# Optimization experiments

Hardware: AMD Instinct MI355X
Metric: run time of the kernel (lower is better)

The kernel has to match this reference:

```python
import jax, jax.numpy as jnp
import numpy as np

BS, SEQ, H = 64, 512, 768
E, T, K = 32, 64, 64


def setup_inputs() -> dict:
    key = jax.random.key(0)
    ks = jax.random.split(key, 16)
    return {
        "hidden_states": jax.random.normal(ks[0], (BS, SEQ, H), dtype=jnp.float32),
        "Wsrc": jax.random.normal(ks[1], (862, 384), dtype=jnp.float32) * 0.02,
        "Wtgt": jax.random.normal(ks[2], (862, 384), dtype=jnp.float32) * 0.02,
        "W_cls": jax.random.normal(ks[3], (2, 6144), dtype=jnp.float32) * 0.02,
        "b_cls": jnp.zeros((2,), dtype=jnp.float32),
        "W_topic": jax.random.normal(ks[4], (2, 6144), dtype=jnp.float32) * 0.02,
        "b_topic": jnp.zeros((2,), dtype=jnp.float32),
        "W_token": jax.random.normal(ks[5], (2, 6144), dtype=jnp.float32) * 0.02,
        "b_token": jnp.zeros((2,), dtype=jnp.float32),
        "source_ids": jax.random.randint(ks[6], (BS,), 0, 862),
        "target_ids": jax.random.randint(ks[7], (BS,), 0, 862),
        "ent_inds": jax.random.randint(ks[8], (BS, E), 0, SEQ - 1),
        "ent_mask": jnp.ones((BS, E), dtype=jnp.float32),
        "topic_inds": jax.random.randint(ks[9], (BS, T), 0, SEQ),
        "topic_mask": jnp.ones((BS, T), dtype=jnp.float32),
        "token_inds": jax.random.randint(ks[10], (BS, K), 0, SEQ),
        "token_mask": jnp.ones((BS, K), dtype=jnp.float32),
    }


def reference(hidden_states, Wsrc, Wtgt, W_cls, b_cls, W_topic, b_topic,
              W_token, b_token, source_ids, target_ids, ent_inds, ent_mask,
              topic_inds, topic_mask, token_inds, token_mask):
    bs = hidden_states.shape[0]
    # domain embedding: concat(source_emb, target_emb) -> [bs, 768] -> [bs, 96, 8]
    domain = jnp.concatenate([Wsrc[source_ids], Wtgt[target_ids]], axis=1)
    d0 = domain.reshape(bs, 96, 8)

    def gather(inds, mask, offset=0):
        # ragged gather of hidden states at token positions, zero-padded slots masked
        h = jnp.take_along_axis(hidden_states, (inds + offset)[:, :, None], axis=1)
        return h * mask[:, :, None]  # [bs, L, 768]

    ent_h = gather(ent_inds, ent_mask, offset=1)
    topic_h = gather(topic_inds, topic_mask)
    token_h = gather(token_inds, token_mask)

    # CLS bilinear: outer product over the 8-dim factor, [bs,96,8,8] -> [bs,6144]
    cls_h = hidden_states[:, 0, :].reshape(bs, 96, 8)
    bl_cls = (d0[:, :, :, None] * cls_h[:, :, None, :]).reshape(bs, 6144)
    cls_logits = jax.nn.softmax(bl_cls @ W_cls.T + b_cls, axis=1)

    def bilin(h, W, b):
        h4 = h.reshape(bs, -1, 96, 8)  # [bs, L, 96, 8]
        bl = (d0[:, None, :, :, None] * h4[:, :, :, None, :]).reshape(bs, h4.shape[1], 6144)
        return bl @ W.T + b  # [bs, L, n_out]

    topic_logits = jax.nn.softmax(bilin(topic_h, W_topic, b_topic), axis=2)
    token_logits = bilin(token_h, W_token, b_token)
    return cls_logits, topic_logits, token_logits
```

## Files before the change

### kernel.cpp

```cpp
#include <hip/hip_runtime.h>

#define BSZ 64
#define SEQ 512
#define HD  768
#define TT  64
#define NROW 6
#define NTASK 129

__global__ __launch_bounds__(256) void compute_V_kernel(
    const float* __restrict__ Wsrc,
    const float* __restrict__ Wtgt,
    const float* __restrict__ W_cls,
    const float* __restrict__ W_topic,
    const float* __restrict__ W_token,
    const int*   __restrict__ source_ids,
    const int*   __restrict__ target_ids,
    float*       __restrict__ Vg)
{
    __shared__ __align__(16) float dom[HD];
    const int b   = blockIdx.x;
    const int tid = threadIdx.x;

    const int sid = source_ids[b];
    const int tgt = target_ids[b];
    for (int j = tid; j < HD; j += 256)
        dom[j] = (j < 384) ? Wsrc[sid * 384 + j] : Wtgt[tgt * 384 + (j - 384)];
    __syncthreads();

    for (int idx = tid; idx < NROW * HD; idx += 256) {
        const int r = idx / HD;
        const int d = idx - r * HD;
        const int w = r >> 1, o = r & 1;
        const float* Wp = (w == 0) ? W_cls : (w == 1) ? W_topic : W_token;
        const int m = d >> 3, c = d & 7;
        const float* wrow = Wp + o * 6144 + m * 64 + c;
        float acc = 0.f;
        #pragma unroll
        for (int a = 0; a < 8; ++a)
            acc = fmaf(dom[m * 8 + a], wrow[a * 8], acc);
        Vg[(size_t)b * (NROW * HD) + idx] = acc;
    }
}

__global__ __launch_bounds__(256) void task_kernel(
    const float* __restrict__ hidden,
    const float* __restrict__ Vg,
    const float* __restrict__ b_cls,
    const float* __restrict__ b_topic,
    const float* __restrict__ b_token,
    const int*   __restrict__ topic_inds,
    const float* __restrict__ topic_mask,
    const int*   __restrict__ token_inds,
    const float* __restrict__ token_mask,
    float*       __restrict__ out)
{
    const int wg   = blockIdx.x * 4 + (threadIdx.x >> 6);
    const int lane = threadIdx.x & 63;
    const int b    = wg / NTASK;
    const int t    = wg - b * NTASK;

    int w, pos, outoff;
    float mask;
    const float* bias;
    bool do_softmax;
    if (t == 0) {
        w = 0; pos = 0; mask = 1.f; bias = b_cls; do_softmax = true;
        outoff = b * 2;
    } else if (t <= TT) {
        const int l = t - 1;
        w = 1; pos = topic_inds[b * TT + l]; mask = topic_mask[b * TT + l];
        bias = b_topic; do_softmax = true;
        outoff = 128 + (b * TT + l) * 2;
    } else {
        const int l = t - 1 - TT;
        w = 2; pos = token_inds[b * TT + l]; mask = token_mask[b * TT + l];
        bias = b_token; do_softmax = false;
        outoff = 128 + BSZ * TT * 2 + (b * TT + l) * 2;
    }

    const float4* hrow = reinterpret_cast<const float4*>(
        hidden + ((size_t)b * SEQ + (size_t)pos) * HD);
    const float4* v0 = reinterpret_cast<const float4*>(
        Vg + ((size_t)b * NROW + w * 2 + 0) * HD);
    const float4* v1 = reinterpret_cast<const float4*>(
        Vg + ((size_t)b * NROW + w * 2 + 1) * HD);

    float a0 = 0.f, a1 = 0.f;
    #pragma unroll
    for (int k = 0; k < 3; ++k) {
        const float4 h4 = hrow[lane + k * 64];
        const float4 x0 = v0[lane + k * 64];
        const float4 x1 = v1[lane + k * 64];
        a0 = fmaf(h4.x, x0.x, a0); a1 = fmaf(h4.x, x1.x, a1);
        a0 = fmaf(h4.y, x0.y, a0); a1 = fmaf(h4.y, x1.y, a1);
        a0 = fmaf(h4.z, x0.z, a0); a1 = fmaf(h4.z, x1.z, a1);
        a0 = fmaf(h4.w, x0.w, a0); a1 = fmaf(h4.w, x1.w, a1);
    }
    #pragma unroll
    for (int off = 32; off > 0; off >>= 1) {
        a0 += __shfl_down(a0, off, 64);
        a1 += __shfl_down(a1, off, 64);
    }

    if (lane == 0) {
        const float l0 = fmaf(mask, a0, bias[0]);
        const float l1 = fmaf(mask, a1, bias[1]);
        if (do_softmax) {
            const float mx = fmaxf(l0, l1);
            const float e0 = __expf(l0 - mx);
            const float e1 = __expf(l1 - mx);
            const float inv = 1.f / (e0 + e1);
            out[outoff]     = e0 * inv;
            out[outoff + 1] = e1 * inv;
        } else {
            out[outoff]     = l0;
            out[outoff + 1] = l1;
        }
    }
}

extern "C" void kernel_launch(void* const* d_in, const int* in_sizes, int n_in,
                              void* d_out, int out_size, void* d_ws, size_t ws_size,
                              hipStream_t stream) {
    const float* hidden     = (const float*)d_in[0];
    const float* Wsrc       = (const float*)d_in[1];
    const float* Wtgt       = (const float*)d_in[2];
    const float* W_cls      = (const float*)d_in[3];
    const float* b_cls      = (const float*)d_in[4];
    const float* W_topic    = (const float*)d_in[5];
    const float* b_topic    = (const float*)d_in[6];
    const float* W_token    = (const float*)d_in[7];
    const float* b_token    = (const float*)d_in[8];
    const int*   source_ids = (const int*)d_in[9];
    const int*   target_ids = (const int*)d_in[10];
    const int*   topic_inds = (const int*)d_in[13];
    const float* topic_mask = (const float*)d_in[14];
    const int*   token_inds = (const int*)d_in[15];
    const float* token_mask = (const float*)d_in[16];
    float* out = (float*)d_out;
    float* Vg  = (float*)d_ws;

    compute_V_kernel<<<BSZ, 256, 0, stream>>>(
        Wsrc, Wtgt, W_cls, W_topic, W_token, source_ids, target_ids, Vg);

    task_kernel<<<(BSZ * NTASK) / 4, 256, 0, stream>>>(
        hidden, Vg, b_cls, b_topic, b_token,
        topic_inds, topic_mask, token_inds, token_mask, out);
}
```

Measured before the change: 168.1 us.

## Fuse V computation and task dot-products into one kernel with shared-memory V

Merges the two kernels into a single launch of 512 blocks (8 partitions per batch item). Each block recomputes only the V rows it needs into shared memory, then runs its 16 or 17 gather-dot tasks against LDS instead of a global workspace. This removes one kernel launch, the global V write and read-back, and the serialisation between the two kernels. In exchange, V rows are computed redundantly across partitions and only 512 blocks exist versus the previous 2064, so there is less parallelism.

```diff
diff --git a/kernel.cpp b/kernel.cpp
--- a/kernel.cpp
+++ b/kernel.cpp
@@ -4,21 +4,33 @@
 #define SEQ 512
 #define HD  768
 #define TT  64
-#define NROW 6
-#define NTASK 129
+#define NPART 8
+#define TPP 16
 
-__global__ __launch_bounds__(256) void compute_V_kernel(
+__global__ __launch_bounds__(256) void fused_kernel(
+    const float* __restrict__ hidden,
     const float* __restrict__ Wsrc,
     const float* __restrict__ Wtgt,
     const float* __restrict__ W_cls,
     const float* __restrict__ W_topic,
     const float* __restrict__ W_token,
+    const float* __restrict__ b_cls,
+    const float* __restrict__ b_topic,
+    const float* __restrict__ b_token,
     const int*   __restrict__ source_ids,
     const int*   __restrict__ target_ids,
-    float*       __restrict__ Vg)
+    const int*   __restrict__ topic_inds,
+    const float* __restrict__ topic_mask,
+    const int*   __restrict__ token_inds,
+    const float* __restrict__ token_mask,
+    float*       __restrict__ out)
 {
     __shared__ __align__(16) float dom[HD];
-    const int b   = blockIdx.x;
+    __shared__ __align__(16) float Vl[4][HD];
+
+    const int blk = blockIdx.x;
+    const int b   = blk >> 3;
+    const int p   = blk & 7;
     const int tid = threadIdx.x;
 
     const int sid = source_ids[b];
@@ -27,10 +39,16 @@
         dom[j] = (j < 384) ? Wsrc[sid * 384 + j] : Wtgt[tgt * 384 + (j - 384)];
     __syncthreads();
 
-    for (int idx = tid; idx < NROW * HD; idx += 256) {
-        const int r = idx / HD;
-        const int d = idx - r * HD;
-        const int w = r >> 1, o = r & 1;
+    int base_row, nrows;
+    if (p == 0)      { base_row = 0; nrows = 4; }
+    else if (p < 4)  { base_row = 2; nrows = 2; }
+    else             { base_row = 4; nrows = 2; }
+
+    for (int idx = tid; idx < nrows * HD; idx += 256) {
+        const int ri = idx / HD;
+        const int d  = idx - ri * HD;
+        const int r  = base_row + ri;
+        const int w  = r >> 1, o = r & 1;
         const float* Wp = (w == 0) ? W_cls : (w == 1) ? W_topic : W_token;
         const int m = d >> 3, c = d & 7;
         const float* wrow = Wp + o * 6144 + m * 64 + c;
@@ -38,83 +56,72 @@
         #pragma unroll
         for (int a = 0; a < 8; ++a)
             acc = fmaf(dom[m * 8 + a], wrow[a * 8], acc);
-        Vg[(size_t)b * (NROW * HD) + idx] = acc;
+        Vl[ri][d] = acc;
     }
-}
+    __syncthreads();
 
-__global__ __launch_bounds__(256) void task_kernel(
-    const float* __restrict__ hidden,
-    const float* __restrict__ Vg,
-    const float* __restrict__ b_cls,
-    const float* __restrict__ b_topic,
-    const float* __restrict__ b_token,
-    const int*   __restrict__ topic_inds,
-    const float* __restrict__ topic_mask,
-    const int*   __restrict__ token_inds,
-    const float* __restrict__ token_mask,
-    float*       __restrict__ out)
-{
-    const int wg   = blockIdx.x * 4 + (threadIdx.x >> 6);
-    const int lane = threadIdx.x & 63;
-    const int b    = wg / NTASK;
-    const int t    = wg - b * NTASK;
+    const int wid  = tid >> 6;
+    const int lane = tid & 63;
+    const int ntasks = (p == 0) ? (1 + TPP) : TPP;
 
-    int w, pos, outoff;
-    float mask;
-    const float* bias;
-    bool do_softmax;
-    if (t == 0) {
-        w = 0; pos = 0; mask = 1.f; bias = b_cls; do_softmax = true;
-        outoff = b * 2;
-    } else if (t <= TT) {
-        const int l = t - 1;
-        w = 1; pos = topic_inds[b * TT + l]; mask = topic_mask[b * TT + l];
-        bias = b_topic; do_softmax = true;
-        outoff = 128 + (b * TT + l) * 2;
-    } else {
-        const int l = t - 1 - TT;
-        w = 2; pos = token_inds[b * TT + l]; mask = token_mask[b * TT + l];
-        bias = b_token; do_softmax = false;
-        outoff = 128 + BSZ * TT * 2 + (b * TT + l) * 2;
-    }
+    for (int ti = wid; ti < ntasks; ti += 4) {
+        int pos, outoff, vbase;
+        float mask;
+        const float* bias;
+        bool do_softmax;
+        if (p == 0 && ti == 0) {
+            pos = 0; mask = 1.f; bias = b_cls; do_softmax = true;
+            outoff = b * 2; vbase = 0;
+        } else if (p < 4) {
+            const int l = (p == 0) ? (ti - 1) : (p * TPP + ti);
+            pos = topic_inds[b * TT + l]; mask = topic_mask[b * TT + l];
+            bias = b_topic; do_softmax = true;
+            outoff = 128 + (b * TT + l) * 2;
+            vbase = (p == 0) ? 2 : 0;
+        } else {
+            const int l = (p - 4) * TPP + ti;
+            pos = token_inds[b * TT + l]; mask = token_mask[b * TT + l];
+            bias = b_token; do_softmax = false;
+            outoff = 128 + BSZ * TT * 2 + (b * TT + l) * 2;
+            vbase = 0;
+        }
 
-    const float4* hrow = reinterpret_cast<const float4*>(
-        hidden + ((size_t)b * SEQ + (size_t)pos) * HD);
-    const float4* v0 = reinterpret_cast<const float4*>(
-        Vg + ((size_t)b * NROW + w * 2 + 0) * HD);
-    const float4* v1 = reinterpret_cast<const float4*>(
-        Vg + ((size_t)b * NROW + w * 2 + 1) * HD);
+        const float4* hrow = reinterpret_cast<const float4*>(
+            hidden + ((size_t)b * SEQ + (size_t)pos) * HD);
+        const float4* v0 = reinterpret_cast<const float4*>(&Vl[vbase][0]);
+        const float4* v1 = reinterpret_cast<const float4*>(&Vl[vbase + 1][0]);
 
-    float a0 = 0.f, a1 = 0.f;
-    #pragma unroll
-    for (int k = 0; k < 3; ++k) {
-        const float4 h4 = hrow[lane + k * 64];
-        const float4 x0 = v0[lane + k * 64];
-        const float4 x1 = v1[lane + k * 64];
-        a0 = fmaf(h4.x, x0.x, a0); a1 = fmaf(h4.x, x1.x, a1);
-        a0 = fmaf(h4.y, x0.y, a0); a1 = fmaf(h4.y, x1.y, a1);
-        a0 = fmaf(h4.z, x0.z, a0); a1 = fmaf(h4.z, x1.z, a1);
-        a0 = fmaf(h4.w, x0.w, a0); a1 = fmaf(h4.w, x1.w, a1);
-    }
-    #pragma unroll
-    for (int off = 32; off > 0; off >>= 1) {
-        a0 += __shfl_down(a0, off, 64);
-        a1 += __shfl_down(a1, off, 64);
-    }
+        float a0 = 0.f, a1 = 0.f;
+        #pragma unroll
+        for (int k = 0; k < 3; ++k) {
+            const float4 h4 = hrow[lane + k * 64];
+            const float4 x0 = v0[lane + k * 64];
+            const float4 x1 = v1[lane + k * 64];
+            a0 = fmaf(h4.x, x0.x, a0); a1 = fmaf(h4.x, x1.x, a1);
+            a0 = fmaf(h4.y, x0.y, a0); a1 = fmaf(h4.y, x1.y, a1);
+            a0 = fmaf(h4.z, x0.z, a0); a1 = fmaf(h4.z, x1.z, a1);
+            a0 = fmaf(h4.w, x0.w, a0); a1 = fmaf(h4.w, x1.w, a1);
+        }
+        #pragma unroll
+        for (int off = 32; off > 0; off >>= 1) {
+            a0 += __shfl_down(a0, off, 64);
+            a1 += __shfl_down(a1, off, 64);
+        }
 
-    if (lane == 0) {
-        const float l0 = fmaf(mask, a0, bias[0]);
-        const float l1 = fmaf(mask, a1, bias[1]);
-        if (do_softmax) {
-            const float mx = fmaxf(l0, l1);
-            const float e0 = __expf(l0 - mx);
-            const float e1 = __expf(l1 - mx);
-            const float inv = 1.f / (e0 + e1);
-            out[outoff]     = e0 * inv;
-            out[outoff + 1] = e1 * inv;
-        } else {
-            out[outoff]     = l0;
-            out[outoff + 1] = l1;
+        if (lane == 0) {
+            const float l0 = fmaf(mask, a0, bias[0]);
+            const float l1 = fmaf(mask, a1, bias[1]);
+            if (do_softmax) {
+                const float mx = fmaxf(l0, l1);
+                const float e0 = __expf(l0 - mx);
+                const float e1 = __expf(l1 - mx);
+                const float inv = 1.f / (e0 + e1);
+                out[outoff]     = e0 * inv;
+                out[outoff + 1] = e1 * inv;
+            } else {
+                out[outoff]     = l0;
+                out[outoff + 1] = l1;
+            }
         }
     }
 }
@@ -138,12 +145,9 @@
     const int*   token_inds = (const int*)d_in[15];
     const float* token_mask = (const float*)d_in[16];
     float* out = (float*)d_out;
-    float* Vg  = (float*)d_ws;
 
-    compute_V_kernel<<<BSZ, 256, 0, stream>>>(
-        Wsrc, Wtgt, W_cls, W_topic, W_token, source_ids, target_ids, Vg);
-
-    task_kernel<<<(BSZ * NTASK) / 4, 256, 0, stream>>>(
-        hidden, Vg, b_cls, b_topic, b_token,
+    fused_kernel<<<BSZ * NPART, 256, 0, stream>>>(
+        hidden, Wsrc, Wtgt, W_cls, W_topic, W_token,
+        b_cls, b_topic, b_token, source_ids, target_ids,
         topic_inds, topic_mask, token_inds, token_mask, out);
 }
```

Result: no change. 165.9 us (median of 2 runs) (-1.3%).
